# Optimization experiments

Hardware: AMD Instinct MI355X
Metric: run time of the kernel (lower is better)

## Reference

```python
import jax, jax.numpy as jnp
import numpy as np

N_SRC = 32768   # source-type nodes
N_DST = 32768   # predict-type nodes
N = N_SRC + N_DST
E = 524288      # pos-graph edges (src-type -> predict-type)
E_NEG = 419430
D_IN = 256
D_H = 256
EPS = 1e-8      # torch cosine_similarity eps


def setup_inputs() -> dict:
    key = jax.random.key(0)
    ks = jax.random.split(key, 6)
    feat = jax.random.normal(ks[0], (N, D_IN), jnp.float32)
    src = jax.random.randint(ks[1], (E,), 0, N_SRC, jnp.int32)
    dst = jax.random.randint(ks[2], (E,), 0, N_DST, jnp.int32) + N_SRC  # edges into predict partition
    perm = jax.random.permutation(ks[3], E)[:E_NEG]  # drop-edge fuse
    neg_src = src[perm]
    neg_dst = dst[perm]
    W = jax.random.normal(ks[4], (D_IN, D_H), jnp.float32) / np.float32(np.sqrt(D_IN))
    b = jnp.zeros((D_H,), jnp.float32)
    prelu_a = jnp.full((1,), 0.25, jnp.float32)  # PReLU default init
    return {"feat": feat, "src": src, "dst": dst, "neg_src": neg_src,
            "neg_dst": neg_dst, "W": W, "b": b, "prelu_a": prelu_a}


def _graph_conv(feat, src, dst, W, b, a):
    # DGL GraphConv(norm='right') on homogeneous graph with self-loops added:
    # h_v = PReLU( (sum_{u->v} x_u W) / in_deg(v) + b )
    loop = jnp.arange(N, dtype=src.dtype)
    s = jnp.concatenate([src, loop])
    d = jnp.concatenate([dst, loop])
    m = feat @ W                                   # [N, D_H]
    agg = jax.ops.segment_sum(m[s], d, num_segments=N)
    deg = jax.ops.segment_sum(jnp.ones_like(d, m.dtype), d, num_segments=N)
    h = agg / jnp.maximum(deg, 1.0)[:, None] + b
    return jnp.where(h >= 0, h, a * h)             # PReLU (single shared slope)


def _normalize(x):
    n = jnp.maximum(jnp.linalg.norm(x, axis=-1, keepdims=True), EPS)
    return x / n


def _seg_cos(anchor_n, nei_n, s, d):
    # per-edge cosine(anchor[dst], nei[src]) summed over in-edges of each predict node
    c = jnp.sum(anchor_n[d] * nei_n[s], axis=-1)
    mask = d >= N_SRC
    idx = jnp.where(mask, d - N_SRC, 0)
    return jax.ops.segment_sum(jnp.where(mask, c, jnp.zeros_like(c)), idx, num_segments=N_DST)


def reference(feat, src, dst, neg_src, neg_dst, W, b, prelu_a):
    h_pos = _graph_conv(feat, src, dst, W, b, prelu_a)
    h_neg = _graph_conv(feat, neg_src, neg_dst, W, b, prelu_a)
    hp = _normalize(h_pos)
    hn = _normalize(h_neg)
    # positive pairs: same predict node across the two views
    pos_loss = jnp.sum(hp[N_SRC:] * hn[N_SRC:], axis=-1)  # [N_DST]
    # neighbor sets include the self-loop (dgl.add_self_loop before the loss)
    loop = jnp.arange(N, dtype=src.dtype)
    ps, pd = jnp.concatenate([src, loop]), jnp.concatenate([dst, loop])
    ns, nd = jnp.concatenate([neg_src, loop]), jnp.concatenate([neg_dst, loop])
    neg_loss = jnp.concatenate([
        _seg_cos(hp, hn, ns, nd),   # pos anchors vs neg-graph in-neighbors
        _seg_cos(hn, hp, ps, pd),   # neg anchors vs pos-graph in-neighbors
    ])
    all_sim = jnp.concatenate([pos_loss, neg_loss])
    loss = jnp.log(jnp.sum(jnp.exp(all_sim))) - jnp.sum(pos_loss)
    return loss, h_pos[N_SRC:]
```

## Files before the change

kernel.cpp:

```cpp
#include <hip/hip_runtime.h>
#include <math.h>

#define NSRC 32768
#define NTOT 65536
#define NDST 32768
#define DH   256
#define SLOTS 64

typedef __attribute__((ext_vector_type(8))) short bf16x8;
typedef __attribute__((ext_vector_type(4))) float f32x4;

__device__ __forceinline__ float wave_reduce(float v) {
#pragma unroll
  for (int off = 32; off > 0; off >>= 1) v += __shfl_xor(v, off, 64);
  return v;
}
__device__ __forceinline__ unsigned short f2bf(float f) {
  union { float f; unsigned u; } v; v.f = f;
  unsigned r = v.u + 0x7FFFu + ((v.u >> 16) & 1u);
  return (unsigned short)(r >> 16);
}
__device__ __forceinline__ float bf2f(unsigned short h) {
  union { unsigned u; float f; } v; v.u = ((unsigned)h) << 16;
  return v.f;
}
__device__ __forceinline__ float4 bf4(ushort4 v) {
  return make_float4(bf2f(v.x), bf2f(v.y), bf2f(v.z), bf2f(v.w));
}
__device__ __forceinline__ void add4(float4& a, const float4 v) {
  a.x += v.x; a.y += v.y; a.z += v.z; a.w += v.w;
}
__device__ __forceinline__ float4 sub4(const float4 a, const float4 v) {
  return make_float4(a.x - v.x, a.y - v.y, a.z - v.z, a.w - v.w);
}
__device__ __forceinline__ float dot4(const float4 a, const float4 b) {
  return a.x * b.x + a.y * b.y + a.z * b.z + a.w * b.w;
}
__device__ __forceinline__ float4 hsrc4(const float4 v, const float4 bv,
                                        float alpha, float isc) {
  float4 h;
  h.x = v.x + bv.x; h.x = (h.x >= 0.f ? h.x : alpha * h.x) * isc;
  h.y = v.y + bv.y; h.y = (h.y >= 0.f ? h.y : alpha * h.y) * isc;
  h.z = v.z + bv.z; h.z = (h.z >= 0.f ? h.z : alpha * h.z) * isc;
  h.w = v.w + bv.w; h.w = (h.w >= 0.f ? h.w : alpha * h.w) * isc;
  return h;
}

__global__ __launch_bounds__(256) void k_prep(const float* __restrict__ W,
                                              unsigned short* __restrict__ Wt,
                                              const int* __restrict__ src,
                                              const int* __restrict__ dst,
                                              const int* __restrict__ ndst,
                                              int* __restrict__ cur,
                                              int* __restrict__ eSrc,
                                              int* __restrict__ degN,
                                              int nE, int nEn) {
  int bid = blockIdx.x;
  const int t = threadIdx.x;
  if (bid < 256) {
    Wt[bid * 256 + t] = f2bf(W[(size_t)t * 256 + bid]);
    return;
  }
  bid -= 256;
  const int nbP = (nE + 255) / 256;
  if (bid < nbP) {
    const int e = bid * 256 + t;
    if (e < nE) {
      const int d = dst[e] - NSRC;
      const int p = atomicAdd(&cur[d], 1);
      if (p < SLOTS) eSrc[d * SLOTS + p] = src[e];
    }
    return;
  }
  bid -= nbP;
  const int e = bid * 256 + t;
  if (e < nEn) atomicAdd(&degN[ndst[e] - NSRC], 1);
}

__global__ __launch_bounds__(512) void k_gemm_mfma(
    const float* __restrict__ A, const unsigned short* __restrict__ Wt,
    const float* __restrict__ b, const float* __restrict__ pa,
    unsigned short* __restrict__ mb, float* __restrict__ inn) {
  __shared__ unsigned short wl[16384];
  const int bid = blockIdx.x;
  const int t = threadIdx.x;
  const int lane = t & 63;
  const int wv = t >> 6;
  const int ln = lane & 15;
  const int kq = lane >> 4;
  const int row = bid * 128 + wv * 16 + ln;
  const bool is_src = (bid < 256);
  const float alpha = pa[0];

  bf16x8 bs[8];
  const float* ap = A + (size_t)row * 256 + kq * 8;
#pragma unroll
  for (int ks = 0; ks < 8; ++ks) {
    float4 a0 = *(const float4*)(ap + ks * 32);
    float4 a1 = *(const float4*)(ap + ks * 32 + 4);
    bf16x8 v;
    v[0] = (short)f2bf(a0.x); v[1] = (short)f2bf(a0.y);
    v[2] = (short)f2bf(a0.z); v[3] = (short)f2bf(a0.w);
    v[4] = (short)f2bf(a1.x); v[5] = (short)f2bf(a1.y);
    v[6] = (short)f2bf(a1.z); v[7] = (short)f2bf(a1.w);
    bs[ks] = v;
  }

  float ss = 0.f;
  for (int q = 0; q < 4; ++q) {
    __syncthreads();
#pragma unroll
    for (int r = 0; r < 4; ++r) {
      const int flat = r * 512 + t;
      const int f = flat >> 6;
      const int ls = flat & 63;
      const int n = q * 64 + (f >> 3) * 16 + (ls & 15);
      const int k = ((ls >> 4) << 3) + (f & 7) * 32;
      *(bf16x8*)(wl + flat * 8) = *(const bf16x8*)(Wt + (size_t)n * 256 + k);
    }
    __syncthreads();

    f32x4 acc[4];
#pragma unroll
    for (int i = 0; i < 4; ++i) acc[i] = (f32x4){0.f, 0.f, 0.f, 0.f};
#pragma unroll
    for (int nt = 0; nt < 4; ++nt) {
#pragma unroll
      for (int ks = 0; ks < 8; ++ks) {
        bf16x8 af = *(const bf16x8*)(wl + ((nt * 8 + ks) * 64 + lane) * 8);
        acc[nt] = __builtin_amdgcn_mfma_f32_16x16x32_bf16(af, bs[ks], acc[nt], 0, 0, 0);
      }
    }
    const int n0 = q * 64 + kq * 4;
#pragma unroll
    for (int nt = 0; nt < 4; ++nt) {
      ushort4 o;
      o.x = f2bf(acc[nt][0]); o.y = f2bf(acc[nt][1]);
      o.z = f2bf(acc[nt][2]); o.w = f2bf(acc[nt][3]);
      *(ushort4*)(mb + (size_t)row * 256 + n0 + nt * 16) = o;
      if (is_src) {
        float4 bv = *(const float4*)(b + n0 + nt * 16);
        float hx = acc[nt][0] + bv.x; hx = hx >= 0.f ? hx : alpha * hx;
        float hy = acc[nt][1] + bv.y; hy = hy >= 0.f ? hy : alpha * hy;
        float hz = acc[nt][2] + bv.z; hz = hz >= 0.f ? hz : alpha * hz;
        float hw = acc[nt][3] + bv.w; hw = hw >= 0.f ? hw : alpha * hw;
        ss += hx * hx + hy * hy + hz * hz + hw * hw;
      }
    }
  }
  if (is_src) {
    ss += __shfl_xor(ss, 16, 64);
    ss += __shfl_xor(ss, 32, 64);
    if (kq == 0) inn[row] = 1.0f / fmaxf(sqrtf(ss), 1e-8f);
  }
}

__global__ __launch_bounds__(256) void k_claim(const int* __restrict__ nsrc,
                                               const int* __restrict__ ndst,
                                               const int* __restrict__ cur,
                                               const int* __restrict__ eSrc,
                                               int* __restrict__ claim, int nEn) {
  const int i = blockIdx.x * 256 + threadIdx.x;
  if (i >= nEn) return;
  const int d = ndst[i] - NSRC;
  const int s = nsrc[i];
  const int cnt = cur[d];
  const int base = d * SLOTS;
  for (int j = 0; j < cnt; ++j) {
    if (eSrc[base + j] == s) {
      if (atomicCAS(&claim[base + j], 0, 1) == 0) return;
    }
  }
}

__global__ __launch_bounds__(256) void k_fused(const unsigned short* __restrict__ mb,
                                               const float* __restrict__ inn,
                                               const int* __restrict__ cur,
                                               const int* __restrict__ eSrc,
                                               const int* __restrict__ claim,
                                               const int* __restrict__ degN,
                                               const float* __restrict__ b,
                                               const float* __restrict__ pa,
                                               float* __restrict__ hraw,
                                               float* __restrict__ sims) {
  const int row = blockIdx.x * 4 + (threadIdx.x >> 6);
  const int lane = threadIdx.x & 63;
  const int c = lane * 4;
  const int cnt = cur[row];
  const int base = row * SLOTS;
  const int cN = degN[row];
  const float4 bv = *(const float4*)(b + c);
  const float alpha = pa[0];

  float4 self = bf4(*(const ushort4*)(mb + (size_t)(NSRC + row) * 256 + c));
  float4 aP0 = self, aP1 = {0.f, 0.f, 0.f, 0.f};
  float4 sP0 = {0.f, 0.f, 0.f, 0.f}, sP1 = {0.f, 0.f, 0.f, 0.f};
  float4 aU0 = {0.f, 0.f, 0.f, 0.f}, aU1 = {0.f, 0.f, 0.f, 0.f};
  float4 sU0 = {0.f, 0.f, 0.f, 0.f}, sU1 = {0.f, 0.f, 0.f, 0.f};

  int e = 0;
  for (; e + 3 < cnt; e += 4) {
    const int s0 = eSrc[base + e],     s1 = eSrc[base + e + 1];
    const int s2 = eSrc[base + e + 2], s3 = eSrc[base + e + 3];
    ushort4 r0 = *(const ushort4*)(mb + (size_t)s0 * 256 + c);
    ushort4 r1 = *(const ushort4*)(mb + (size_t)s1 * 256 + c);
    ushort4 r2 = *(const ushort4*)(mb + (size_t)s2 * 256 + c);
    ushort4 r3 = *(const ushort4*)(mb + (size_t)s3 * 256 + c);
    const int cl0 = claim[base + e],     cl1 = claim[base + e + 1];
    const int cl2 = claim[base + e + 2], cl3 = claim[base + e + 3];
    const float i0 = inn[s0], i1 = inn[s1], i2 = inn[s2], i3 = inn[s3];
    float4 v0 = bf4(r0), v1 = bf4(r1), v2 = bf4(r2), v3 = bf4(r3);
    float4 h0 = hsrc4(v0, bv, alpha, i0);
    float4 h1 = hsrc4(v1, bv, alpha, i1);
    float4 h2 = hsrc4(v2, bv, alpha, i2);
    float4 h3 = hsrc4(v3, bv, alpha, i3);
    add4(aP0, v0); add4(aP1, v1); add4(aP0, v2); add4(aP1, v3);
    add4(sP0, h0); add4(sP1, h1); add4(sP0, h2); add4(sP1, h3);
    if (!cl0) { add4(aU0, v0); add4(sU0, h0); }
    if (!cl1) { add4(aU1, v1); add4(sU1, h1); }
    if (!cl2) { add4(aU0, v2); add4(sU0, h2); }
    if (!cl3) { add4(aU1, v3); add4(sU1, h3); }
  }
  for (; e < cnt; ++e) {
    const int s0 = eSrc[base + e];
    const int cl0 = claim[base + e];
    const float i0 = inn[s0];
    float4 v0 = bf4(*(const ushort4*)(mb + (size_t)s0 * 256 + c));
    float4 h0 = hsrc4(v0, bv, alpha, i0);
    add4(aP0, v0); add4(sP0, h0);
    if (!cl0) { add4(aU0, v0); add4(sU0, h0); }
  }
  add4(aP0, aP1); add4(sP0, sP1); add4(aU0, aU1); add4(sU0, sU1);
  float4 aN0 = sub4(aP0, aU0);
  float4 sN0 = sub4(sP0, sU0);

  const float invP = 1.0f / (float)(cnt + 1);
  const float invN = 1.0f / (float)(cN + 1);
  float4 hp, hn;
  hp.x = aP0.x * invP + bv.x; hp.x = hp.x >= 0.f ? hp.x : alpha * hp.x;
  hp.y = aP0.y * invP + bv.y; hp.y = hp.y >= 0.f ? hp.y : alpha * hp.y;
  hp.z = aP0.z * invP + bv.z; hp.z = hp.z >= 0.f ? hp.z : alpha * hp.z;
  hp.w = aP0.w * invP + bv.w; hp.w = hp.w >= 0.f ? hp.w : alpha * hp.w;
  hn.x = aN0.x * invN + bv.x; hn.x = hn.x >= 0.f ? hn.x : alpha * hn.x;
  hn.y = aN0.y * invN + bv.y; hn.y = hn.y >= 0.f ? hn.y : alpha * hn.y;
  hn.z = aN0.z * invN + bv.z; hn.z = hn.z >= 0.f ? hn.z : alpha * hn.z;
  hn.w = aN0.w * invN + bv.w; hn.w = hn.w >= 0.f ? hn.w : alpha * hn.w;

  *(float4*)(hraw + (size_t)row * 256 + c) = hp;

  float ssP = wave_reduce(dot4(hp, hp));
  float ssN = wave_reduce(dot4(hn, hn));
  const float iP = 1.0f / fmaxf(sqrtf(ssP), 1e-8f);
  const float iN = 1.0f / fmaxf(sqrtf(ssN), 1e-8f);
  float4 xp = hp, xn = hn;
  xp.x *= iP; xp.y *= iP; xp.z *= iP; xp.w *= iP;
  xn.x *= iN; xn.y *= iN; xn.z *= iN; xn.w *= iN;

  float pos = wave_reduce(dot4(xp, xn));
  float n1 = wave_reduce(dot4(xp, sN0));
  float n2 = wave_reduce(dot4(xn, sP0));
  if (lane == 0) {
    sims[row] = pos;
    sims[NDST + row] = pos + n1;
    sims[2 * NDST + row] = pos + n2;
  }
}

__global__ __launch_bounds__(256) void k_reduce(const float* __restrict__ sims,
                                                float* __restrict__ red) {
  const int i = blockIdx.x * 256 + threadIdx.x;
  const float v = sims[i];
  float e = expf(v);
  float p = (i < NDST) ? v : 0.f;
  e = wave_reduce(e);
  p = wave_reduce(p);
  __shared__ float se[4], sp[4];
  const int lane = threadIdx.x & 63, w = threadIdx.x >> 6;
  if (lane == 0) { se[w] = e; sp[w] = p; }
  __syncthreads();
  if (threadIdx.x == 0) {
    atomicAdd(red + 0, se[0] + se[1] + se[2] + se[3]);
    atomicAdd(red + 1, sp[0] + sp[1] + sp[2] + sp[3]);
  }
}

__global__ void k_final(const float* __restrict__ red, float* __restrict__ out) {
  out[0] = logf(red[0]) - red[1];
}

extern "C" void kernel_launch(void* const* d_in, const int* in_sizes, int n_in,
                              void* d_out, int out_size, void* d_ws, size_t ws_size,
                              hipStream_t stream) {
  const float* feat = (const float*)d_in[0];
  const int*   src  = (const int*)d_in[1];
  const int*   dst  = (const int*)d_in[2];
  const int*   nsrc = (const int*)d_in[3];
  const int*   ndst = (const int*)d_in[4];
  const float* W    = (const float*)d_in[5];
  const float* b    = (const float*)d_in[6];
  const float* pa   = (const float*)d_in[7];
  const int nE  = in_sizes[1];
  const int nEn = in_sizes[3];
  float* out = (float*)d_out;

  unsigned short* mb = (unsigned short*)d_ws;
  unsigned short* Wt = mb + (size_t)NTOT * 256;
  float* inn  = (float*)(Wt + 256 * 256);
  float* sims = inn + NSRC;
  int* eSrc = (int*)(sims + 3 * (size_t)NDST);
  int* cur  = eSrc + (size_t)NDST * SLOTS;
  int* degN = cur + NDST;
  float* red = (float*)(degN + NDST);
  int* claim = (int*)(red + 8);
  const size_t zero_bytes = (2 * (size_t)NDST + 8 + (size_t)NDST * SLOTS) * 4;

  hipMemsetAsync(cur, 0, zero_bytes, stream);

  const int nbP = (nE + 255) / 256, nbN = (nEn + 255) / 256;
  k_prep<<<256 + nbP + nbN, 256, 0, stream>>>(W, Wt, src, dst, ndst, cur, eSrc,
                                              degN, nE, nEn);
  k_gemm_mfma<<<512, 512, 0, stream>>>(feat, Wt, b, pa, mb, inn);
  k_claim<<<nbN, 256, 0, stream>>>(nsrc, ndst, cur, eSrc, claim, nEn);
  k_fused<<<NDST / 4, 256, 0, stream>>>(mb, inn, cur, eSrc, claim, degN, b, pa,
                                        out + 1, sims);
  k_reduce<<<(3 * NDST) / 256, 256, 0, stream>>>(sims, red);
  k_final<<<1, 1, 0, stream>>>(red, out);
}
```

Before: 188.4 us.

## Store projected features as fp8, fuse claim into GEMM, fold final into reduce

The projected feature matrix is now stored as packed fp8 instead of bf16, halving the bytes gathered per edge in the aggregation kernel. The claim-matching pass becomes extra blocks of the GEMM launch. The large claim-array memset is replaced by zeroing only the written slots in the prep kernel. The final log-sum is computed by the last block of the reduction via a ticket counter, removing a launch. fp8 storage loses considerable precision in h_pos and the loss, which risks exceeding the accuracy tolerance.

```diff
diff --git a/kernel.cpp b/kernel.cpp
--- a/kernel.cpp
+++ b/kernel.cpp
@@ -9,6 +9,7 @@
 
 typedef __attribute__((ext_vector_type(8))) short bf16x8;
 typedef __attribute__((ext_vector_type(4))) float f32x4;
+typedef __attribute__((ext_vector_type(2))) float f32x2;
 
 __device__ __forceinline__ float wave_reduce(float v) {
 #pragma unroll
@@ -20,12 +21,15 @@
   unsigned r = v.u + 0x7FFFu + ((v.u >> 16) & 1u);
   return (unsigned short)(r >> 16);
 }
-__device__ __forceinline__ float bf2f(unsigned short h) {
-  union { unsigned u; float f; } v; v.u = ((unsigned)h) << 16;
-  return v.f;
-}
-__device__ __forceinline__ float4 bf4(ushort4 v) {
-  return make_float4(bf2f(v.x), bf2f(v.y), bf2f(v.z), bf2f(v.w));
+__device__ __forceinline__ unsigned pk_fp8(float x, float y, float z, float w) {
+  int v = __builtin_amdgcn_cvt_pk_fp8_f32(x, y, 0, false);
+  v = __builtin_amdgcn_cvt_pk_fp8_f32(z, w, v, true);
+  return (unsigned)v;
+}
+__device__ __forceinline__ float4 unpk_fp8(unsigned u) {
+  f32x2 lo = __builtin_amdgcn_cvt_pk_f32_fp8((int)u, false);
+  f32x2 hi = __builtin_amdgcn_cvt_pk_f32_fp8((int)u, true);
+  return make_float4(lo[0], lo[1], hi[0], hi[1]);
 }
 __device__ __forceinline__ void add4(float4& a, const float4 v) {
   a.x += v.x; a.y += v.y; a.z += v.z; a.w += v.w;
@@ -53,6 +57,7 @@
                                               const int* __restrict__ ndst,
                                               int* __restrict__ cur,
                                               int* __restrict__ eSrc,
+                                              int* __restrict__ claim,
                                               int* __restrict__ degN,
                                               int nE, int nEn) {
   int bid = blockIdx.x;
@@ -68,7 +73,10 @@
     if (e < nE) {
       const int d = dst[e] - NSRC;
       const int p = atomicAdd(&cur[d], 1);
-      if (p < SLOTS) eSrc[d * SLOTS + p] = src[e];
+      if (p < SLOTS) {
+        eSrc[d * SLOTS + p] = src[e];
+        claim[d * SLOTS + p] = 0;
+      }
     }
     return;
   }
@@ -77,13 +85,32 @@
   if (e < nEn) atomicAdd(&degN[ndst[e] - NSRC], 1);
 }
 
-__global__ __launch_bounds__(512) void k_gemm_mfma(
+__global__ __launch_bounds__(512) void k_gemm_claim(
     const float* __restrict__ A, const unsigned short* __restrict__ Wt,
     const float* __restrict__ b, const float* __restrict__ pa,
-    unsigned short* __restrict__ mb, float* __restrict__ inn) {
+    unsigned* __restrict__ mb8, float* __restrict__ inn,
+    const int* __restrict__ nsrc, const int* __restrict__ ndst,
+    const int* __restrict__ cur, const int* __restrict__ eSrc,
+    int* __restrict__ claim, int nEn) {
   __shared__ unsigned short wl[16384];
   const int bid = blockIdx.x;
   const int t = threadIdx.x;
+
+  if (bid >= 512) {
+    const int i = (bid - 512) * 512 + t;
+    if (i >= nEn) return;
+    const int d = ndst[i] - NSRC;
+    const int s = nsrc[i];
+    const int cnt = cur[d];
+    const int base = d * SLOTS;
+    for (int j = 0; j < cnt; ++j) {
+      if (eSrc[base + j] == s) {
+        if (atomicCAS(&claim[base + j], 0, 1) == 0) return;
+      }
+    }
+    return;
+  }
+
   const int lane = t & 63;
   const int wv = t >> 6;
   const int ln = lane & 15;
@@ -131,15 +158,13 @@
         acc[nt] = __builtin_amdgcn_mfma_f32_16x16x32_bf16(af, bs[ks], acc[nt], 0, 0, 0);
       }
     }
-    const int n0 = q * 64 + kq * 4;
 #pragma unroll
     for (int nt = 0; nt < 4; ++nt) {
-      ushort4 o;
-      o.x = f2bf(acc[nt][0]); o.y = f2bf(acc[nt][1]);
-      o.z = f2bf(acc[nt][2]); o.w = f2bf(acc[nt][3]);
-      *(ushort4*)(mb + (size_t)row * 256 + n0 + nt * 16) = o;
+      mb8[(size_t)row * 64 + q * 16 + nt * 4 + kq] =
+          pk_fp8(acc[nt][0], acc[nt][1], acc[nt][2], acc[nt][3]);
       if (is_src) {
-        float4 bv = *(const float4*)(b + n0 + nt * 16);
+        const int n0 = q * 64 + nt * 16 + kq * 4;
+        float4 bv = *(const float4*)(b + n0);
         float hx = acc[nt][0] + bv.x; hx = hx >= 0.f ? hx : alpha * hx;
         float hy = acc[nt][1] + bv.y; hy = hy >= 0.f ? hy : alpha * hy;
         float hz = acc[nt][2] + bv.z; hz = hz >= 0.f ? hz : alpha * hz;
@@ -155,25 +180,7 @@
   }
 }
 
-__global__ __launch_bounds__(256) void k_claim(const int* __restrict__ nsrc,
-                                               const int* __restrict__ ndst,
-                                               const int* __restrict__ cur,
-                                               const int* __restrict__ eSrc,
-                                               int* __restrict__ claim, int nEn) {
-  const int i = blockIdx.x * 256 + threadIdx.x;
-  if (i >= nEn) return;
-  const int d = ndst[i] - NSRC;
-  const int s = nsrc[i];
-  const int cnt = cur[d];
-  const int base = d * SLOTS;
-  for (int j = 0; j < cnt; ++j) {
-    if (eSrc[base + j] == s) {
-      if (atomicCAS(&claim[base + j], 0, 1) == 0) return;
-    }
-  }
-}
-
-__global__ __launch_bounds__(256) void k_fused(const unsigned short* __restrict__ mb,
+__global__ __launch_bounds__(256) void k_fused(const unsigned* __restrict__ mb8,
                                                const float* __restrict__ inn,
                                                const int* __restrict__ cur,
                                                const int* __restrict__ eSrc,
@@ -192,7 +199,7 @@
   const float4 bv = *(const float4*)(b + c);
   const float alpha = pa[0];
 
-  float4 self = bf4(*(const ushort4*)(mb + (size_t)(NSRC + row) * 256 + c));
+  float4 self = unpk_fp8(mb8[(size_t)(NSRC + row) * 64 + lane]);
   float4 aP0 = self, aP1 = {0.f, 0.f, 0.f, 0.f};
   float4 sP0 = {0.f, 0.f, 0.f, 0.f}, sP1 = {0.f, 0.f, 0.f, 0.f};
   float4 aU0 = {0.f, 0.f, 0.f, 0.f}, aU1 = {0.f, 0.f, 0.f, 0.f};
@@ -202,14 +209,15 @@
   for (; e + 3 < cnt; e += 4) {
     const int s0 = eSrc[base + e],     s1 = eSrc[base + e + 1];
     const int s2 = eSrc[base + e + 2], s3 = eSrc[base + e + 3];
-    ushort4 r0 = *(const ushort4*)(mb + (size_t)s0 * 256 + c);
-    ushort4 r1 = *(const ushort4*)(mb + (size_t)s1 * 256 + c);
-    ushort4 r2 = *(const ushort4*)(mb + (size_t)s2 * 256 + c);
-    ushort4 r3 = *(const ushort4*)(mb + (size_t)s3 * 256 + c);
+    const unsigned r0 = mb8[(size_t)s0 * 64 + lane];
+    const unsigned r1 = mb8[(size_t)s1 * 64 + lane];
+    const unsigned r2 = mb8[(size_t)s2 * 64 + lane];
+    const unsigned r3 = mb8[(size_t)s3 * 64 + lane];
     const int cl0 = claim[base + e],     cl1 = claim[base + e + 1];
     const int cl2 = claim[base + e + 2], cl3 = claim[base + e + 3];
     const float i0 = inn[s0], i1 = inn[s1], i2 = inn[s2], i3 = inn[s3];
-    float4 v0 = bf4(r0), v1 = bf4(r1), v2 = bf4(r2), v3 = bf4(r3);
+    float4 v0 = unpk_fp8(r0), v1 = unpk_fp8(r1);
+    float4 v2 = unpk_fp8(r2), v3 = unpk_fp8(r3);
     float4 h0 = hsrc4(v0, bv, alpha, i0);
     float4 h1 = hsrc4(v1, bv, alpha, i1);
     float4 h2 = hsrc4(v2, bv, alpha, i2);
@@ -225,7 +233,7 @@
     const int s0 = eSrc[base + e];
     const int cl0 = claim[base + e];
     const float i0 = inn[s0];
-    float4 v0 = bf4(*(const ushort4*)(mb + (size_t)s0 * 256 + c));
+    float4 v0 = unpk_fp8(mb8[(size_t)s0 * 64 + lane]);
     float4 h0 = hsrc4(v0, bv, alpha, i0);
     add4(aP0, v0); add4(sP0, h0);
     if (!cl0) { add4(aU0, v0); add4(sU0, h0); }
@@ -267,7 +275,10 @@
 }
 
 __global__ __launch_bounds__(256) void k_reduce(const float* __restrict__ sims,
-                                                float* __restrict__ red) {
+                                                float* __restrict__ red,
+                                                int* __restrict__ ticket,
+                                                float* __restrict__ out,
+                                                int nblocks) {
   const int i = blockIdx.x * 256 + threadIdx.x;
   const float v = sims[i];
   float e = expf(v);
@@ -281,11 +292,14 @@
   if (threadIdx.x == 0) {
     atomicAdd(red + 0, se[0] + se[1] + se[2] + se[3]);
     atomicAdd(red + 1, sp[0] + sp[1] + sp[2] + sp[3]);
-  }
-}
-
-__global__ void k_final(const float* __restrict__ red, float* __restrict__ out) {
-  out[0] = logf(red[0]) - red[1];
+    __threadfence();
+    const int old = atomicAdd(ticket, 1);
+    if (old == nblocks - 1) {
+      const float s = atomicAdd(red + 0, 0.0f);
+      const float q = atomicAdd(red + 1, 0.0f);
+      out[0] = logf(s) - q;
+    }
+  }
 }
 
 extern "C" void kernel_launch(void* const* d_in, const int* in_sizes, int n_in,
@@ -303,26 +317,28 @@
   const int nEn = in_sizes[3];
   float* out = (float*)d_out;
 
-  unsigned short* mb = (unsigned short*)d_ws;
-  unsigned short* Wt = mb + (size_t)NTOT * 256;
+  unsigned* mb8 = (unsigned*)d_ws;
+  unsigned short* Wt = (unsigned short*)(mb8 + (size_t)NTOT * 64);
   float* inn  = (float*)(Wt + 256 * 256);
   float* sims = inn + NSRC;
   int* eSrc = (int*)(sims + 3 * (size_t)NDST);
-  int* cur  = eSrc + (size_t)NDST * SLOTS;
+  int* claim = eSrc + (size_t)NDST * SLOTS;
+  int* cur  = claim + (size_t)NDST * SLOTS;
   int* degN = cur + NDST;
   float* red = (float*)(degN + NDST);
-  int* claim = (int*)(red + 8);
-  const size_t zero_bytes = (2 * (size_t)NDST + 8 + (size_t)NDST * SLOTS) * 4;
+  int* ticket = (int*)(red + 4);
+  const size_t zero_bytes = (2 * (size_t)NDST + 8) * 4;
 
   hipMemsetAsync(cur, 0, zero_bytes, stream);
 
   const int nbP = (nE + 255) / 256, nbN = (nEn + 255) / 256;
   k_prep<<<256 + nbP + nbN, 256, 0, stream>>>(W, Wt, src, dst, ndst, cur, eSrc,
-                                              degN, nE, nEn);
-  k_gemm_mfma<<<512, 512, 0, stream>>>(feat, Wt, b, pa, mb, inn);
-  k_claim<<<nbN, 256, 0, stream>>>(nsrc, ndst, cur, eSrc, claim, nEn);
-  k_fused<<<NDST / 4, 256, 0, stream>>>(mb, inn, cur, eSrc, claim, degN, b, pa,
+                                              claim, degN, nE, nEn);
+  const int nbC = (nEn + 511) / 512;
+  k_gemm_claim<<<512 + nbC, 512, 0, stream>>>(feat, Wt, b, pa, mb8, inn,
+                                              nsrc, ndst, cur, eSrc, claim, nEn);
+  k_fused<<<NDST / 4, 256, 0, stream>>>(mb8, inn, cur, eSrc, claim, degN, b, pa,
                                         out + 1, sims);
-  k_reduce<<<(3 * NDST) / 256, 256, 0, stream>>>(sims, red);
-  k_final<<<1, 1, 0, stream>>>(red, out);
-}
+  const int nbR = (3 * NDST) / 256;
+  k_reduce<<<nbR, 256, 0, stream>>>(sims, red, ticket, out, nbR);
+}
```

Result: slower. 198.7 us (+5.5%).
